# Optimization experiments

Measured on AMD Instinct MI355X. Metric: run time of the kernel, lower is better.

The kernel has to match this reference:

```python
import jax, jax.numpy as jnp
import numpy as np

N = 20000
E = 320000
F_IN = 50
HID = 64          # hidden_channels
HEADS = 8
WIDTH = HID * HEADS  # 512
NUM_CLASSES = 121


def setup_inputs() -> dict:
    key = jax.random.key(0)
    ks = jax.random.split(key, 16)
    def p(k, shape, fan_in):
        return (jax.random.normal(k, shape, dtype=jnp.float32) / np.sqrt(fan_in)).astype(jnp.float32)
    x = jax.random.normal(ks[0], (N, F_IN), dtype=jnp.float32)
    edge_index = jax.random.randint(ks[1], (2, E), 0, N, dtype=jnp.int64)
    return {
        "x": x,
        "edge_index": edge_index,
        # layer 1: 50 -> 64, heads=8, concat
        "W1": p(ks[2], (F_IN, HEADS * HID), F_IN),
        "a1_src": p(ks[3], (HEADS, HID), HID),
        "a1_dst": p(ks[4], (HEADS, HID), HID),
        "b1": jnp.zeros((HEADS * HID,), jnp.float32),
        # layer 2: 512 -> 512, heads=1, concat
        "W2": p(ks[5], (WIDTH, WIDTH), WIDTH),
        "a2_src": p(ks[6], (1, WIDTH), WIDTH),
        "a2_dst": p(ks[7], (1, WIDTH), WIDTH),
        "b2": jnp.zeros((WIDTH,), jnp.float32),
        # layer 3: 512 -> 121, heads=1, concat=False (mean)
        "W3": p(ks[8], (WIDTH, NUM_CLASSES), WIDTH),
        "a3_src": p(ks[9], (1, NUM_CLASSES), NUM_CLASSES),
        "a3_dst": p(ks[10], (1, NUM_CLASSES), NUM_CLASSES),
        "b3": jnp.zeros((NUM_CLASSES,), jnp.float32),
    }


def gat_conv(x, src, dst, W, a_src, a_dst, b, heads, out_ch, concat):
    n = x.shape[0]
    h = (x @ W).reshape(n, heads, out_ch)                 # [N, H, C]
    al_s = jnp.sum(h * a_src, axis=-1)                     # [N, H]
    al_d = jnp.sum(h * a_dst, axis=-1)                     # [N, H]
    e = jax.nn.leaky_relu(al_s[src] + al_d[dst], 0.2)      # [E, H]
    # edge softmax per destination node (stable)
    m = jax.ops.segment_max(e, dst, num_segments=n)        # [N, H]
    m = jnp.where(jnp.isfinite(m), m, 0.0)
    ex = jnp.exp(e - m[dst])
    z = jax.ops.segment_sum(ex, dst, num_segments=n)       # [N, H]
    alpha = ex / (z[dst] + 1e-16)                          # [E, H]
    msg = h[src] * alpha[..., None]                        # [E, H, C]
    out = jax.ops.segment_sum(msg, dst, num_segments=n)    # [N, H, C]
    out = out.reshape(n, heads * out_ch) if concat else out.mean(axis=1)
    return out + b


def reference(x, edge_index, W1, a1_src, a1_dst, b1, W2, a2_src, a2_dst, b2, W3, a3_src, a3_dst, b3):
    n = x.shape[0]
    # PyG GATConv adds self loops by default
    loops = jnp.arange(n, dtype=edge_index.dtype)
    src = jnp.concatenate([edge_index[0], loops])
    dst = jnp.concatenate([edge_index[1], loops])
    # eval mode: dropout is identity
    x1 = gat_conv(x, src, dst, W1, a1_src, a1_dst, b1, HEADS, HID, True)
    h = jax.nn.elu(x1)
    x1 = gat_conv(h, src, dst, W2, a2_src, a2_dst, b2, 1, WIDTH, True)
    h = jax.nn.elu(x1)
    x1 = gat_conv(h, src, dst, W3, a3_src, a3_dst, b3, 1, NUM_CLASSES, False)
    return x1
```

## Files before the change

kernel.cpp:

```cpp
#include <hip/hip_runtime.h>
#include <hip/hip_bf16.h>
#include <hip/hip_fp16.h>

#define NN     20000
#define ERAW   320000
#define ETOT   (ERAW + NN)
#define F_IN   50
#define HID    64
#define HEADS  8
#define WIDTH  512
#define NCLS   121
#define NCLS_P 128

typedef __attribute__((ext_vector_type(8))) __bf16 bf16x8;
typedef __attribute__((ext_vector_type(4))) float floatx4;

__device__ __forceinline__ unsigned short f32_to_bf16_rn(float f) {
  unsigned u = __float_as_uint(f);
  unsigned r = u + 0x7fffu + ((u >> 16) & 1u);
  return (unsigned short)(r >> 16);
}
__device__ __forceinline__ void split_one(float f, unsigned short& h,
                                          unsigned short& l) {
  h = f32_to_bf16_rn(f);
  float fh = __uint_as_float(((unsigned)h) << 16);
  l = f32_to_bf16_rn(f - fh);
}

__device__ __forceinline__ float2 u2f2(unsigned u) {
  __half2 hv = *reinterpret_cast<__half2*>(&u);
  return __half22float2(hv);
}

__device__ __forceinline__ void gll16(const unsigned short* g,
                                      const unsigned short* l) {
  __builtin_amdgcn_global_load_lds(
      (const __attribute__((address_space(1))) unsigned int*)(const void*)g,
      (__attribute__((address_space(3))) unsigned int*)(void*)l, 16, 0, 0);
}

#define PW_BLOCKS 449
__global__ __launch_bounds__(256) void prep_weights(
    const float* __restrict__ W1, const float* __restrict__ W2,
    const float* __restrict__ W3, const float* __restrict__ a1s,
    const float* __restrict__ a1d, unsigned short* __restrict__ w1hHi,
    unsigned short* __restrict__ w1hLo, unsigned short* __restrict__ w2tHi,
    unsigned short* __restrict__ w2tLo, unsigned short* __restrict__ w3tHi,
    unsigned short* __restrict__ w3tLo, float* __restrict__ w1as,
    float* __restrict__ w1ad) {
  __shared__ float t[32][33];
  const int b = blockIdx.x;
  if (b < 320) {
    const float* W;
    unsigned short *thi, *tlo;
    int M, Mp, bx, by;
    const int K = WIDTH;
    if (b < 256) {
      W = W2; thi = w2tHi; tlo = w2tLo; M = WIDTH; Mp = WIDTH;
      bx = b & 15; by = b >> 4;
    } else {
      int bb = b - 256;
      W = W3; thi = w3tHi; tlo = w3tLo; M = NCLS; Mp = NCLS_P;
      bx = bb & 15; by = bb >> 4;
    }
    int k0 = bx * 32, m0 = by * 32;
    int tx = threadIdx.x & 31, ty = threadIdx.x >> 5;
    #pragma unroll
    for (int r = 0; r < 4; ++r) {
      int k = k0 + ty + r * 8, m = m0 + tx;
      float v = 0.f;
      if (k < K && m < M) v = W[(size_t)k * M + m];
      t[ty + r * 8][tx] = v;
    }
    __syncthreads();
    #pragma unroll
    for (int r = 0; r < 4; ++r) {
      int m = m0 + ty + r * 8, k = k0 + tx;
      if (m < Mp && k < K) {
        unsigned short h, l;
        split_one(t[tx][ty + r * 8], h, l);
        thi[(size_t)m * K + k] = h;
        tlo[(size_t)m * K + k] = l;
      }
    }
  } else if (b < 448) {
    int idx = (b - 320) * 256 + threadIdx.x;
    if (idx < HEADS * HID * HID) {
      int hd = idx >> 12, rem = idx & 4095;
      int col = rem >> 6, k = rem & 63;
      float v = (k < F_IN) ? W1[(size_t)k * WIDTH + hd * HID + col] : 0.f;
      unsigned short h, l;
      split_one(v, h, l);
      w1hHi[idx] = h;
      w1hLo[idx] = l;
    }
  } else {
    for (int idx = threadIdx.x; idx < 2 * F_IN * HEADS; idx += 256) {
      int which = idx >= F_IN * HEADS;
      int r = which ? idx - F_IN * HEADS : idx;
      int k = r >> 3, h = r & 7;
      const float* a = which ? a1d : a1s;
      float s = 0.f;
      for (int c = 0; c < HID; ++c)
        s += W1[(size_t)k * WIDTH + h * HID + c] * a[h * HID + c];
      (which ? w1ad : w1as)[r] = s;
    }
  }
}

template <int MI>
__global__ __launch_bounds__(512) void gemm_split_db(
    const unsigned short* __restrict__ Ahi, const unsigned short* __restrict__ Alo,
    const unsigned short* __restrict__ Bthi, const unsigned short* __restrict__ Btlo,
    __half* __restrict__ C16, int N, int K, int M, int Mp, int RB, int CB) {
  constexpr int ABUF = MI * 2048;
  constexpr int BHALF = MI * 4096;
  constexpr int BUF = MI * 4096 + 16384;
  constexpr int NGW = (MI * 8 + 32) / 8;
  __shared__ unsigned short lds[2 * BUF];

  const int f = blockIdx.x;
  const int xcd = f & 7;
  const int g = f >> 3;
  const int cb = g % CB;
  const int rb = (g / CB) * 8 + xcd;
  if (rb >= RB) return;
  const int r0 = rb * (MI * 32), c0 = cb * 128;

  const int tid = threadIdx.x;
  const int wave = tid >> 6, lane = tid & 63;
  const int wr = wave >> 2, wc = wave & 3;
  const int lkg = lane >> 4, lmn = lane & 15;

  const int row8 = lane >> 3, cslot = lane & 7;
  const unsigned short* gsrc[NGW];
  int ldsoff[NGW];
  #pragma unroll
  for (int i = 0; i < NGW; ++i) {
    int q = wave * NGW + i;
    int a, rg;
    if (q < MI * 4)      { a = 0; rg = q; }
    else if (q < MI * 8) { a = 1; rg = q - MI * 4; }
    else { int qb = q - MI * 8; a = 2 + (qb >> 4); rg = qb & 15; }
    int r = rg * 8 + row8;
    int c = cslot ^ (r & 7);
    const unsigned short* base =
        (a == 0) ? Ahi : (a == 1) ? Alo : (a == 2) ? Bthi : Btlo;
    size_t grow;
    if (a < 2) {
      int ra = r0 + r;
      if (ra > N - 1) ra = N - 1;
      grow = (size_t)ra;
    } else {
      grow = (size_t)(c0 + r);
    }
    gsrc[i] = base + grow * K + c * 8;
    int aoff = (a == 0) ? 0 : (a == 1) ? ABUF : (a == 2) ? BHALF
                                              : (BHALF + 8192);
    ldsoff[i] = aoff + rg * 512;
  }

  int rowA[MI], m7A[MI], rowB[2], m7B[2];
  #pragma unroll
  for (int mi = 0; mi < MI; ++mi) {
    int m = wr * (MI * 16) + mi * 16 + lmn;
    rowA[mi] = m * 64;  m7A[mi] = m & 7;
  }
  #pragma unroll
  for (int ni = 0; ni < 2; ++ni) {
    int n = wc * 32 + ni * 16 + lmn;
    rowB[ni] = BHALF + n * 64;  m7B[ni] = n & 7;
  }

  floatx4 acc[MI][2] = {};

  #pragma unroll
  for (int i = 0; i < NGW; ++i) gll16(gsrc[i], lds + ldsoff[i]);

  const int nk = K >> 6;
  for (int t = 0; t < nk; ++t) {
    if (t + 1 < nk) {
      const unsigned short* dst = lds + ((t + 1) & 1) * BUF;
      #pragma unroll
      for (int i = 0; i < NGW; ++i)
        gll16(gsrc[i] + (t + 1) * 64, dst + ldsoff[i]);
      if constexpr (MI == 4) {
        asm volatile("s_waitcnt vmcnt(8)" ::: "memory");
      } else {
        asm volatile("s_waitcnt vmcnt(6)" ::: "memory");
      }
    } else {
      asm volatile("s_waitcnt vmcnt(0)" ::: "memory");
    }
    __builtin_amdgcn_sched_barrier(0);
    __builtin_amdgcn_s_barrier();
    __builtin_amdgcn_sched_barrier(0);

    const unsigned short* Lb = lds + (t & 1) * BUF;
    #pragma unroll
    for (int ksub = 0; ksub < 2; ++ksub) {
      bf16x8 fAhi[MI], fAlo[MI], fBhi[2], fBlo[2];
      #pragma unroll
      for (int mi = 0; mi < MI; ++mi) {
        int s = rowA[mi] + (((ksub << 2) | lkg) ^ m7A[mi]) * 8;
        fAhi[mi] = *(const bf16x8*)(Lb + s);
        fAlo[mi] = *(const bf16x8*)(Lb + s + ABUF);
      }
      #pragma unroll
      for (int ni = 0; ni < 2; ++ni) {
        int s = rowB[ni] + (((ksub << 2) | lkg) ^ m7B[ni]) * 8;
        fBhi[ni] = *(const bf16x8*)(Lb + s);
        fBlo[ni] = *(const bf16x8*)(Lb + s + 8192);
      }
      #pragma unroll
      for (int mi = 0; mi < MI; ++mi)
        #pragma unroll
        for (int ni = 0; ni < 2; ++ni) {
          acc[mi][ni] = __builtin_amdgcn_mfma_f32_16x16x32_bf16(
              fAhi[mi], fBhi[ni], acc[mi][ni], 0, 0, 0);
          acc[mi][ni] = __builtin_amdgcn_mfma_f32_16x16x32_bf16(
              fAhi[mi], fBlo[ni], acc[mi][ni], 0, 0, 0);
          acc[mi][ni] = __builtin_amdgcn_mfma_f32_16x16x32_bf16(
              fAlo[mi], fBhi[ni], acc[mi][ni], 0, 0, 0);
        }
    }

    __builtin_amdgcn_sched_barrier(0);
    asm volatile("s_waitcnt lgkmcnt(0)" ::: "memory");
    __builtin_amdgcn_s_barrier();
    __builtin_amdgcn_sched_barrier(0);
  }

  #pragma unroll
  for (int mi = 0; mi < MI; ++mi) {
    #pragma unroll
    for (int r = 0; r < 4; ++r) {
      int grow = r0 + wr * (MI * 16) + mi * 16 + lkg * 4 + r;
      if (grow >= N) continue;
      #pragma unroll
      for (int ni = 0; ni < 2; ++ni) {
        int gcol = c0 + wc * 32 + ni * 16 + lmn;
        float v = (gcol < M) ? acc[mi][ni][r] : 0.f;
        C16[(size_t)grow * Mp + gcol] = __float2half(v);
      }
    }
  }
}

__global__ __launch_bounds__(256) void gemm_l1_heads(
    const unsigned short* __restrict__ Ahi, const unsigned short* __restrict__ Alo,
    const unsigned short* __restrict__ Bthi, const unsigned short* __restrict__ Btlo,
    unsigned short* __restrict__ outHi, unsigned short* __restrict__ outLo,
    const float* __restrict__ bias) {
  __shared__ unsigned short sAhi[8192], sAlo[8192], sBhi[4096], sBlo[4096];
  const int tid = threadIdx.x;
  const int wave = tid >> 6, lane = tid & 63;
  const int r0 = blockIdx.x * 128;
  const int hd = blockIdx.y;
  const int lkg = lane >> 4, lmn = lane & 15;

  #pragma unroll
  for (int t = 0; t < 4; ++t) {
    int cid = tid + t * 256;
    int row = cid >> 3, c = cid & 7;
    int gr = r0 + row; if (gr > NN - 1) gr = NN - 1;
    const size_t goff = (size_t)gr * WIDTH + hd * HID + c * 8;
    int loff = (((c >> 2) * 4 + (c & 3)) * 128 + row) * 8;
    *(uint4*)(sAhi + loff) = *(const uint4*)(Ahi + goff);
    *(uint4*)(sAlo + loff) = *(const uint4*)(Alo + goff);
  }
  #pragma unroll
  for (int t = 0; t < 2; ++t) {
    int cid = tid + t * 256;
    int col = cid >> 3, c = cid & 7;
    const size_t goff = (size_t)(hd * HID + col) * HID + c * 8;
    int loff = (((c >> 2) * 4 + (c & 3)) * 64 + col) * 8;
    *(uint4*)(sBhi + loff) = *(const uint4*)(Bthi + goff);
    *(uint4*)(sBlo + loff) = *(const uint4*)(Btlo + goff);
  }
  __syncthreads();

  floatx4 acc[2][4] = {};
  #pragma unroll
  for (int ks = 0; ks < 2; ++ks) {
    bf16x8 fAhi[2], fAlo[2], fBhi[4], fBlo[4];
    #pragma unroll
    for (int mi = 0; mi < 2; ++mi) {
      int m = wave * 32 + mi * 16 + lmn;
      int off = ((ks * 4 + lkg) * 128 + m) * 8;
      fAhi[mi] = *(const bf16x8*)(sAhi + off);
      fAlo[mi] = *(const bf16x8*)(sAlo + off);
    }
    #pragma unroll
    for (int ni = 0; ni < 4; ++ni) {
      int n = ni * 16 + lmn;
      int off = ((ks * 4 + lkg) * 64 + n) * 8;
      fBhi[ni] = *(const bf16x8*)(sBhi + off);
      fBlo[ni] = *(const bf16x8*)(sBlo + off);
    }
    #pragma unroll
    for (int mi = 0; mi < 2; ++mi)
      #pragma unroll
      for (int ni = 0; ni < 4; ++ni) {
        acc[mi][ni] = __builtin_amdgcn_mfma_f32_16x16x32_bf16(
            fAhi[mi], fBhi[ni], acc[mi][ni], 0, 0, 0);
        acc[mi][ni] = __builtin_amdgcn_mfma_f32_16x16x32_bf16(
            fAhi[mi], fBlo[ni], acc[mi][ni], 0, 0, 0);
        acc[mi][ni] = __builtin_amdgcn_mfma_f32_16x16x32_bf16(
            fAlo[mi], fBhi[ni], acc[mi][ni], 0, 0, 0);
      }
  }

  #pragma unroll
  for (int mi = 0; mi < 2; ++mi) {
    #pragma unroll
    for (int r = 0; r < 4; ++r) {
      int grow = r0 + wave * 32 + mi * 16 + (lane >> 4) * 4 + r;
      if (grow >= NN) continue;
      #pragma unroll
      for (int ni = 0; ni < 4; ++ni) {
        int gcol = hd * HID + ni * 16 + lmn;
        float v = acc[mi][ni][r] + bias[gcol];
        v = (v > 0.f) ? v : (__expf(v) - 1.0f);
        unsigned short hh, ll;
        split_one(v, hh, ll);
        outHi[(size_t)grow * WIDTH + gcol] = hh;
        outLo[(size_t)grow * WIDTH + gcol] = ll;
      }
    }
  }
}

__global__ __launch_bounds__(256) void al1_kernel(
    const float* __restrict__ x, const float* __restrict__ w1as,
    const float* __restrict__ w1ad, float* __restrict__ al_s,
    float* __restrict__ al_d) {
  int n = (blockIdx.x * blockDim.x + threadIdx.x) >> 6;
  int lane = threadIdx.x & 63;
  if (n >= NN) return;
  float xv = (lane < F_IN) ? x[(size_t)n * F_IN + lane] : 0.f;
  float ws[HEADS], wd[HEADS];
  #pragma unroll
  for (int h = 0; h < HEADS; ++h) {
    ws[h] = (lane < F_IN) ? w1as[lane * HEADS + h] : 0.f;
    wd[h] = (lane < F_IN) ? w1ad[lane * HEADS + h] : 0.f;
  }
  #pragma unroll
  for (int h = 0; h < HEADS; ++h) {
    float ss = xv * ws[h], sd = xv * wd[h];
    #pragma unroll
    for (int o = 32; o; o >>= 1) {
      ss += __shfl_xor(ss, o);
      sd += __shfl_xor(sd, o);
    }
    if (lane == 0) {
      al_s[n * HEADS + h] = ss;
      al_d[n * HEADS + h] = sd;
    }
  }
}

template <int C, int CS>
__global__ __launch_bounds__(256) void compute_al16(
    const __half* __restrict__ h16, const float* __restrict__ a_src,
    const float* __restrict__ a_dst, float* __restrict__ al_s,
    float* __restrict__ al_d) {
  int n = (blockIdx.x * blockDim.x + threadIdx.x) >> 6;
  int lane = threadIdx.x & 63;
  if (n >= NN) return;
  const __half* hr = h16 + (size_t)n * CS;
  float ss = 0.f, sd = 0.f;
  if (C % 512 == 0) {
    uint4 raw = *(const uint4*)(hr + lane * 8);
    float f[8];
    float2 t;
    t = u2f2(raw.x); f[0] = t.x; f[1] = t.y;
    t = u2f2(raw.y); f[2] = t.x; f[3] = t.y;
    t = u2f2(raw.z); f[4] = t.x; f[5] = t.y;
    t = u2f2(raw.w); f[6] = t.x; f[7] = t.y;
    #pragma unroll
    for (int j = 0; j < 8; ++j) {
      int c = lane * 8 + j;
      ss += f[j] * a_src[c];
      sd += f[j] * a_dst[c];
    }
  } else {
    for (int c = lane; c < C; c += 64) {
      float v = __half2float(hr[c]);
      ss += v * a_src[c];
      sd += v * a_dst[c];
    }
  }
  #pragma unroll
  for (int o = 32; o; o >>= 1) {
    ss += __shfl_xor(ss, o);
    sd += __shfl_xor(sd, o);
  }
  if (lane == 0) {
    al_s[n] = ss;
    al_d[n] = sd;
  }
}

__global__ __launch_bounds__(256) void count_deg(
    const int* __restrict__ edst, int* __restrict__ deg) {
  int e = blockIdx.x * blockDim.x + threadIdx.x;
  if (e >= ETOT) return;
  int d = (e < ERAW) ? edst[e] : (e - ERAW);
  atomicAdd(&deg[d], 1);
}

__global__ __launch_bounds__(1024) void scan_deg(
    const int* __restrict__ deg, int* __restrict__ rowptr) {
  __shared__ int part[1024];
  const int t = threadIdx.x;
  const int CHUNK = (NN + 1023) / 1024;
  int lo = t * CHUNK, hi = min(lo + CHUNK, NN);
  int s = 0;
  for (int i = lo; i < hi; ++i) s += deg[i];
  part[t] = s;
  __syncthreads();
  for (int off = 1; off < 1024; off <<= 1) {
    int v = (t >= off) ? part[t - off] : 0;
    __syncthreads();
    part[t] += v;
    __syncthreads();
  }
  int base = (t == 0) ? 0 : part[t - 1];
  for (int i = lo; i < hi; ++i) {
    rowptr[i] = base;
    base += deg[i];
  }
  if (t == 1023) rowptr[NN] = part[1023];
}

__global__ __launch_bounds__(256) void scatter_csr(
    const int* __restrict__ esrc, const int* __restrict__ edst,
    const int* __restrict__ rowptr, int* __restrict__ cnt,
    int* __restrict__ csrc) {
  int e = blockIdx.x * blockDim.x + threadIdx.x;
  if (e >= ETOT) return;
  int s, d;
  if (e < ERAW) { s = esrc[e]; d = edst[e]; }
  else          { s = e - ERAW; d = e - ERAW; }
  int pos = rowptr[d] + atomicAdd(&cnt[d], 1);
  csrc[pos] = s;
}

__global__ __launch_bounds__(256) void agg_x_sm(
    const int* __restrict__ rowptr, const int* __restrict__ csrc,
    const float* __restrict__ al_s, const float* __restrict__ al_d,
    const float* __restrict__ x, unsigned short* __restrict__ outHi,
    unsigned short* __restrict__ outLo) {
  const int w = threadIdx.x >> 6, lane = threadIdx.x & 63;
  const int d = blockIdx.x * 4 + w;
  if (d >= NN) return;
  const int r0 = rowptr[d], r1 = rowptr[d + 1];
  const int mh = lane & 7;
  const float ald_my = al_d[d * HEADS + mh];
  float m_my = al_s[d * HEADS + mh] + ald_my;
  m_my = (m_my > 0.f) ? m_my : 0.2f * m_my;

  float z_my = 0.f;
  float acc[HEADS];
  #pragma unroll
  for (int hh = 0; hh < HEADS; ++hh) acc[hh] = 0.f;

  int p = r0;
  for (; p + 8 <= r1; p += 8) {
    int s[8];
    #pragma unroll
    for (int j = 0; j < 8; ++j) s[j] = csrc[p + j];
    float xv[8];
    #pragma unroll
    for (int j = 0; j < 8; ++j)
      xv[j] = (lane < F_IN) ? x[(size_t)s[j] * F_IN + lane] : 0.f;
    float av[8];
    #pragma unroll
    for (int j = 0; j < 8; ++j) av[j] = al_s[s[j] * HEADS + mh];
    #pragma unroll
    for (int j = 0; j < 8; ++j) {
      float v = av[j] + ald_my;
      v = (v > 0.f) ? v : 0.2f * v;
      float a = __expf(v - m_my);
      z_my += a;
      #pragma unroll
      for (int hh = 0; hh < HEADS; ++hh) acc[hh] += __shfl(a, hh, 8) * xv[j];
    }
  }
  for (; p < r1; ++p) {
    int s = csrc[p];
    float v = al_s[s * HEADS + mh] + ald_my;
    v = (v > 0.f) ? v : 0.2f * v;
    float a = __expf(v - m_my);
    z_my += a;
    float xv = (lane < F_IN) ? x[(size_t)s * F_IN + lane] : 0.f;
    #pragma unroll
    for (int hh = 0; hh < HEADS; ++hh) acc[hh] += __shfl(a, hh, 8) * xv;
  }

  #pragma unroll
  for (int hh = 0; hh < HEADS; ++hh) {
    float zh = __shfl(z_my, hh, 8);
    float v = (lane < F_IN) ? acc[hh] / (zh + 1e-16f) : 0.f;
    unsigned short h2, l2;
    split_one(v, h2, l2);
    outHi[(size_t)d * WIDTH + hh * HID + lane] = h2;
    outLo[(size_t)d * WIDTH + hh * HID + lane] = l2;
  }
}

template <int M, int MS, bool ELU, bool SPLIT>
__global__ __launch_bounds__(256) void pull_agg_sm(
    const int* __restrict__ rowptr, const int* __restrict__ csrc,
    const float* __restrict__ al_s, const float* __restrict__ al_d,
    const __half* __restrict__ h16, const float* __restrict__ bias,
    float* __restrict__ out, unsigned short* __restrict__ outHi,
    unsigned short* __restrict__ outLo) {
  constexpr int EPL = MS / 64;
  const int w = threadIdx.x >> 6;
  const int lane = threadIdx.x & 63;
  const int d = blockIdx.x * 4 + w;
  if (d >= NN) return;
  const int r0 = rowptr[d], r1 = rowptr[d + 1];
  const float ald = al_d[d];
  float m = al_s[d] + ald;
  m = (m > 0.f) ? m : 0.2f * m;

  const int base = lane * EPL;
  const __half* hb = h16 + base;
  float acc[EPL];
  #pragma unroll
  for (int j = 0; j < EPL; ++j) acc[j] = 0.f;
  float z = 0.f;

  int p = r0;
  for (; p + 8 <= r1; p += 8) {
    int s[8];
    #pragma unroll
    for (int j = 0; j < 8; ++j) s[j] = csrc[p + j];
    uint4 raw8[8];
    unsigned raw2[8];
    #pragma unroll
    for (int j = 0; j < 8; ++j) {
      const __half* hr = hb + (size_t)s[j] * MS;
      if (EPL == 8)      raw8[j] = *(const uint4*)hr;
      else if (EPL == 2) raw2[j] = *(const unsigned*)hr;
    }
    float av[8];
    #pragma unroll
    for (int j = 0; j < 8; ++j) av[j] = al_s[s[j]];
    #pragma unroll
    for (int j = 0; j < 8; ++j) {
      float v = av[j] + ald;
      v = (v > 0.f) ? v : 0.2f * v;
      float a = __expf(v - m);
      z += a;
      if (EPL == 8) {
        float2 f0 = u2f2(raw8[j].x), f1 = u2f2(raw8[j].y);
        float2 f2 = u2f2(raw8[j].z), f3 = u2f2(raw8[j].w);
        acc[0] += f0.x * a; acc[1] += f0.y * a;
        acc[2] += f1.x * a; acc[3] += f1.y * a;
        acc[4] += f2.x * a; acc[5] += f2.y * a;
        acc[6] += f3.x * a; acc[7] += f3.y * a;
      } else if (EPL == 2) {
        float2 f0 = u2f2(raw2[j]);
        acc[0] += f0.x * a;
        acc[1] += f0.y * a;
      }
    }
  }
  for (; p < r1; ++p) {
    int s = csrc[p];
    float v = al_s[s] + ald;
    v = (v > 0.f) ? v : 0.2f * v;
    float a = __expf(v - m);
    z += a;
    const __half* hr = hb + (size_t)s * MS;
    if (EPL == 8) {
      uint4 raw = *(const uint4*)hr;
      float2 f0 = u2f2(raw.x), f1 = u2f2(raw.y);
      float2 f2 = u2f2(raw.z), f3 = u2f2(raw.w);
      acc[0] += f0.x * a; acc[1] += f0.y * a;
      acc[2] += f1.x * a; acc[3] += f1.y * a;
      acc[4] += f2.x * a; acc[5] += f2.y * a;
      acc[6] += f3.x * a; acc[7] += f3.y * a;
    } else if (EPL == 2) {
      unsigned raw = *(const unsigned*)hr;
      float2 f0 = u2f2(raw);
      acc[0] += f0.x * a;
      acc[1] += f0.y * a;
    }
  }
  const float iz = 1.0f / (z + 1e-16f);

  #pragma unroll
  for (int j = 0; j < EPL; ++j) {
    if ((M == MS) || (base + j < M)) {
      float v = acc[j] * iz + bias[base + j];
      if (ELU) v = (v > 0.f) ? v : (__expf(v) - 1.0f);
      if (SPLIT) {
        unsigned short hh, ll;
        split_one(v, hh, ll);
        outHi[(size_t)d * M + base + j] = hh;
        outLo[(size_t)d * M + base + j] = ll;
      } else {
        out[(size_t)d * M + base + j] = v;
      }
    }
  }
}

extern "C" void kernel_launch(void* const* d_in, const int* in_sizes, int n_in,
                              void* d_out, int out_size, void* d_ws,
                              size_t ws_size, hipStream_t stream) {
  const float* x      = (const float*)d_in[0];
  const int*   ei     = (const int*)d_in[1];
  const float* W1     = (const float*)d_in[2];
  const float* a1_src = (const float*)d_in[3];
  const float* a1_dst = (const float*)d_in[4];
  const float* b1     = (const float*)d_in[5];
  const float* W2     = (const float*)d_in[6];
  const float* a2_src = (const float*)d_in[7];
  const float* a2_dst = (const float*)d_in[8];
  const float* b2     = (const float*)d_in[9];
  const float* W3     = (const float*)d_in[10];
  const float* a3_src = (const float*)d_in[11];
  const float* a3_dst = (const float*)d_in[12];
  const float* b3     = (const float*)d_in[13];
  float* out = (float*)d_out;

  const int* esrc = ei;
  const int* edst = ei + ERAW;

  unsigned short* p1Hi  = (unsigned short*)d_ws;
  unsigned short* p1Lo  = p1Hi + (size_t)NN * WIDTH;
  unsigned short* p2Hi  = p1Lo + (size_t)NN * WIDTH;
  unsigned short* p2Lo  = p2Hi + (size_t)NN * WIDTH;
  __half*        h16    = (__half*)(p2Lo + (size_t)NN * WIDTH);
  unsigned short* w1hHi = (unsigned short*)(h16 + (size_t)NN * WIDTH);
  unsigned short* w1hLo = w1hHi + (size_t)HEADS * HID * HID;
  unsigned short* w2tHi = w1hLo + (size_t)HEADS * HID * HID;
  unsigned short* w2tLo = w2tHi + (size_t)WIDTH * WIDTH;
  unsigned short* w3tHi = w2tLo + (size_t)WIDTH * WIDTH;
  unsigned short* w3tLo = w3tHi + (size_t)NCLS_P * WIDTH;
  float* al_s   = (float*)(w3tLo + (size_t)NCLS_P * WIDTH);
  float* al_d   = al_s + (size_t)NN * HEADS;
  float* w1as   = al_d + (size_t)NN * HEADS;
  float* w1ad   = w1as + F_IN * HEADS;
  int* deg      = (int*)(w1ad + F_IN * HEADS);
  int* cnt      = deg + NN;
  int* rowptr   = cnt + NN;
  int* csrc     = rowptr + NN + 4;

  hipMemsetAsync(deg, 0, (size_t)(2 * NN) * sizeof(int), stream);
  const int eblk = (ETOT + 255) / 256;
  count_deg<<<eblk, 256, 0, stream>>>(edst, deg);
  scan_deg<<<1, 1024, 0, stream>>>(deg, rowptr);
  scatter_csr<<<eblk, 256, 0, stream>>>(esrc, edst, rowptr, cnt, csrc);

  prep_weights<<<PW_BLOCKS, 256, 0, stream>>>(
      W1, W2, W3, a1_src, a1_dst, w1hHi, w1hLo, w2tHi, w2tLo, w3tHi, w3tLo,
      w1as, w1ad);

  const int nwblk = (NN + 3) / 4;

  al1_kernel<<<nwblk, 256, 0, stream>>>(x, w1as, w1ad, al_s, al_d);
  agg_x_sm<<<nwblk, 256, 0, stream>>>(rowptr, csrc, al_s, al_d, x, p1Hi,
                                      p1Lo);
  gemm_l1_heads<<<dim3((NN + 127) / 128, HEADS), 256, 0, stream>>>(
      p1Hi, p1Lo, w1hHi, w1hLo, p2Hi, p2Lo, b1);

  const int RB2 = (NN + 127) / 128;
  const int G2 = ((RB2 + 7) / 8) * 8 * (WIDTH / 128);
  gemm_split_db<4><<<G2, 512, 0, stream>>>(
      p2Hi, p2Lo, w2tHi, w2tLo, h16, NN, WIDTH, WIDTH, WIDTH, RB2,
      WIDTH / 128);
  compute_al16<WIDTH, WIDTH><<<nwblk, 256, 0, stream>>>(h16, a2_src, a2_dst,
                                                        al_s, al_d);
  pull_agg_sm<WIDTH, WIDTH, true, true><<<nwblk, 256, 0, stream>>>(
      rowptr, csrc, al_s, al_d, h16, b2, nullptr, p1Hi, p1Lo);

  const int RB3 = (NN + 63) / 64;
  const int G3 = ((RB3 + 7) / 8) * 8 * (NCLS_P / 128);
  gemm_split_db<2><<<G3, 512, 0, stream>>>(
      p1Hi, p1Lo, w3tHi, w3tLo, h16, NN, WIDTH, NCLS, NCLS_P, RB3,
      NCLS_P / 128);
  compute_al16<NCLS, NCLS_P><<<nwblk, 256, 0, stream>>>(h16, a3_src, a3_dst,
                                                        al_s, al_d);
  pull_agg_sm<NCLS, NCLS_P, false, false><<<nwblk, 256, 0, stream>>>(
      rowptr, csrc, al_s, al_d, h16, b3, out, nullptr, nullptr);
}
```

Measured before the change: 390.6 us.

## Pad edge loops to batches of 8 and split final aggregation into half-wave rows

The scalar remainder loops in the three pull-aggregation kernels are replaced by a masked batch of 8, with indices clamped to the last edge and weights zeroed, so every neighbor gather is issued in a batched, unrolled group. The templated aggregation kernel is split into a wide variant for layer 2 and a narrow variant for layer 3. The narrow variant maps two destination nodes per wavefront, 32 lanes each with 4 halves per lane, where the old version used 2 per lane. This doubles the destinations handled per wave and cuts idle lanes for the 128-wide output. Masked tail slots cost redundant loads and exp evaluations.

```diff
diff --git a/kernel.cpp b/kernel.cpp
--- a/kernel.cpp
+++ b/kernel.cpp
@@ -466,11 +466,13 @@
   #pragma unroll
   for (int hh = 0; hh < HEADS; ++hh) acc[hh] = 0.f;
 
-  int p = r0;
-  for (; p + 8 <= r1; p += 8) {
+  for (int p = r0; p < r1; p += 8) {
     int s[8];
     #pragma unroll
-    for (int j = 0; j < 8; ++j) s[j] = csrc[p + j];
+    for (int j = 0; j < 8; ++j) {
+      int pj = p + j; if (pj > r1 - 1) pj = r1 - 1;
+      s[j] = csrc[pj];
+    }
     float xv[8];
     #pragma unroll
     for (int j = 0; j < 8; ++j)
@@ -483,20 +485,11 @@
       float v = av[j] + ald_my;
       v = (v > 0.f) ? v : 0.2f * v;
       float a = __expf(v - m_my);
+      if (p + j >= r1) a = 0.f;
       z_my += a;
       #pragma unroll
       for (int hh = 0; hh < HEADS; ++hh) acc[hh] += __shfl(a, hh, 8) * xv[j];
     }
-  }
-  for (; p < r1; ++p) {
-    int s = csrc[p];
-    float v = al_s[s * HEADS + mh] + ald_my;
-    v = (v > 0.f) ? v : 0.2f * v;
-    float a = __expf(v - m_my);
-    z_my += a;
-    float xv = (lane < F_IN) ? x[(size_t)s * F_IN + lane] : 0.f;
-    #pragma unroll
-    for (int hh = 0; hh < HEADS; ++hh) acc[hh] += __shfl(a, hh, 8) * xv;
   }
 
   #pragma unroll
@@ -510,14 +503,11 @@
   }
 }
 
-template <int M, int MS, bool ELU, bool SPLIT>
-__global__ __launch_bounds__(256) void pull_agg_sm(
+__global__ __launch_bounds__(256) void pull_agg_w(
     const int* __restrict__ rowptr, const int* __restrict__ csrc,
     const float* __restrict__ al_s, const float* __restrict__ al_d,
     const __half* __restrict__ h16, const float* __restrict__ bias,
-    float* __restrict__ out, unsigned short* __restrict__ outHi,
-    unsigned short* __restrict__ outLo) {
-  constexpr int EPL = MS / 64;
+    unsigned short* __restrict__ outHi, unsigned short* __restrict__ outLo) {
   const int w = threadIdx.x >> 6;
   const int lane = threadIdx.x & 63;
   const int d = blockIdx.x * 4 + w;
@@ -527,26 +517,24 @@
   float m = al_s[d] + ald;
   m = (m > 0.f) ? m : 0.2f * m;
 
-  const int base = lane * EPL;
+  const int base = lane * 8;
   const __half* hb = h16 + base;
-  float acc[EPL];
-  #pragma unroll
-  for (int j = 0; j < EPL; ++j) acc[j] = 0.f;
+  float acc[8];
+  #pragma unroll
+  for (int j = 0; j < 8; ++j) acc[j] = 0.f;
   float z = 0.f;
 
-  int p = r0;
-  for (; p + 8 <= r1; p += 8) {
+  for (int p = r0; p < r1; p += 8) {
     int s[8];
     #pragma unroll
-    for (int j = 0; j < 8; ++j) s[j] = csrc[p + j];
+    for (int j = 0; j < 8; ++j) {
+      int pj = p + j; if (pj > r1 - 1) pj = r1 - 1;
+      s[j] = csrc[pj];
+    }
     uint4 raw8[8];
-    unsigned raw2[8];
-    #pragma unroll
-    for (int j = 0; j < 8; ++j) {
-      const __half* hr = hb + (size_t)s[j] * MS;
-      if (EPL == 8)      raw8[j] = *(const uint4*)hr;
-      else if (EPL == 2) raw2[j] = *(const unsigned*)hr;
-    }
+    #pragma unroll
+    for (int j = 0; j < 8; ++j)
+      raw8[j] = *(const uint4*)(hb + (size_t)s[j] * WIDTH);
     float av[8];
     #pragma unroll
     for (int j = 0; j < 8; ++j) av[j] = al_s[s[j]];
@@ -555,59 +543,81 @@
       float v = av[j] + ald;
       v = (v > 0.f) ? v : 0.2f * v;
       float a = __expf(v - m);
+      if (p + j >= r1) a = 0.f;
       z += a;
-      if (EPL == 8) {
-        float2 f0 = u2f2(raw8[j].x), f1 = u2f2(raw8[j].y);
-        float2 f2 = u2f2(raw8[j].z), f3 = u2f2(raw8[j].w);
-        acc[0] += f0.x * a; acc[1] += f0.y * a;
-        acc[2] += f1.x * a; acc[3] += f1.y * a;
-        acc[4] += f2.x * a; acc[5] += f2.y * a;
-        acc[6] += f3.x * a; acc[7] += f3.y * a;
-      } else if (EPL == 2) {
-        float2 f0 = u2f2(raw2[j]);
-        acc[0] += f0.x * a;
-        acc[1] += f0.y * a;
-      }
-    }
-  }
-  for (; p < r1; ++p) {
-    int s = csrc[p];
-    float v = al_s[s] + ald;
-    v = (v > 0.f) ? v : 0.2f * v;
-    float a = __expf(v - m);
-    z += a;
-    const __half* hr = hb + (size_t)s * MS;
-    if (EPL == 8) {
-      uint4 raw = *(const uint4*)hr;
-      float2 f0 = u2f2(raw.x), f1 = u2f2(raw.y);
-      float2 f2 = u2f2(raw.z), f3 = u2f2(raw.w);
+      float2 f0 = u2f2(raw8[j].x), f1 = u2f2(raw8[j].y);
+      float2 f2 = u2f2(raw8[j].z), f3 = u2f2(raw8[j].w);
       acc[0] += f0.x * a; acc[1] += f0.y * a;
       acc[2] += f1.x * a; acc[3] += f1.y * a;
       acc[4] += f2.x * a; acc[5] += f2.y * a;
       acc[6] += f3.x * a; acc[7] += f3.y * a;
-    } else if (EPL == 2) {
-      unsigned raw = *(const unsigned*)hr;
-      float2 f0 = u2f2(raw);
-      acc[0] += f0.x * a;
-      acc[1] += f0.y * a;
     }
   }
   const float iz = 1.0f / (z + 1e-16f);
 
   #pragma unroll
-  for (int j = 0; j < EPL; ++j) {
-    if ((M == MS) || (base + j < M)) {
-      float v = acc[j] * iz + bias[base + j];
-      if (ELU) v = (v > 0.f) ? v : (__expf(v) - 1.0f);
-      if (SPLIT) {
-        unsigned short hh, ll;
-        split_one(v, hh, ll);
-        outHi[(size_t)d * M + base + j] = hh;
-        outLo[(size_t)d * M + base + j] = ll;
-      } else {
-        out[(size_t)d * M + base + j] = v;
-      }
-    }
+  for (int j = 0; j < 8; ++j) {
+    float v = acc[j] * iz + bias[base + j];
+    v = (v > 0.f) ? v : (__expf(v) - 1.0f);
+    unsigned short hh, ll;
+    split_one(v, hh, ll);
+    outHi[(size_t)d * WIDTH + base + j] = hh;
+    outLo[(size_t)d * WIDTH + base + j] = ll;
+  }
+}
+
+__global__ __launch_bounds__(256) void pull_agg_n(
+    const int* __restrict__ rowptr, const int* __restrict__ csrc,
+    const float* __restrict__ al_s, const float* __restrict__ al_d,
+    const __half* __restrict__ h16, const float* __restrict__ bias,
+    float* __restrict__ out) {
+  const int w = threadIdx.x >> 6, lane = threadIdx.x & 63;
+  const int half = lane >> 5, li = lane & 31;
+  const int d = blockIdx.x * 8 + w * 2 + half;
+  if (d >= NN) return;
+  const int r0 = rowptr[d], r1 = rowptr[d + 1];
+  const float ald = al_d[d];
+  float m = al_s[d] + ald;
+  m = (m > 0.f) ? m : 0.2f * m;
+
+  const int base = li * 4;
+  const __half* hb = h16 + base;
+  float acc[4] = {0.f, 0.f, 0.f, 0.f};
+  float z = 0.f;
+
+  for (int p = r0; p < r1; p += 8) {
+    int s[8];
+    #pragma unroll
+    for (int j = 0; j < 8; ++j) {
+      int pj = p + j; if (pj > r1 - 1) pj = r1 - 1;
+      s[j] = csrc[pj];
+    }
+    uint2 raw[8];
+    #pragma unroll
+    for (int j = 0; j < 8; ++j)
+      raw[j] = *(const uint2*)(hb + (size_t)s[j] * NCLS_P);
+    float av[8];
+    #pragma unroll
+    for (int j = 0; j < 8; ++j) av[j] = al_s[s[j]];
+    #pragma unroll
+    for (int j = 0; j < 8; ++j) {
+      float v = av[j] + ald;
+      v = (v > 0.f) ? v : 0.2f * v;
+      float a = __expf(v - m);
+      if (p + j >= r1) a = 0.f;
+      z += a;
+      float2 f0 = u2f2(raw[j].x), f1 = u2f2(raw[j].y);
+      acc[0] += f0.x * a; acc[1] += f0.y * a;
+      acc[2] += f1.x * a; acc[3] += f1.y * a;
+    }
+  }
+  const float iz = 1.0f / (z + 1e-16f);
+
+  #pragma unroll
+  for (int j = 0; j < 4; ++j) {
+    int col = base + j;
+    if (col < NCLS)
+      out[(size_t)d * NCLS + col] = acc[j] * iz + bias[col];
   }
 }
 
@@ -678,8 +688,8 @@
       WIDTH / 128);
   compute_al16<WIDTH, WIDTH><<<nwblk, 256, 0, stream>>>(h16, a2_src, a2_dst,
                                                         al_s, al_d);
-  pull_agg_sm<WIDTH, WIDTH, true, true><<<nwblk, 256, 0, stream>>>(
-      rowptr, csrc, al_s, al_d, h16, b2, nullptr, p1Hi, p1Lo);
+  pull_agg_w<<<nwblk, 256, 0, stream>>>(rowptr, csrc, al_s, al_d, h16, b2,
+                                        p1Hi, p1Lo);
 
   const int RB3 = (NN + 63) / 64;
   const int G3 = ((RB3 + 7) / 8) * 8 * (NCLS_P / 128);
@@ -688,6 +698,6 @@
       NCLS_P / 128);
   compute_al16<NCLS, NCLS_P><<<nwblk, 256, 0, stream>>>(h16, a3_src, a3_dst,
                                                         al_s, al_d);
-  pull_agg_sm<NCLS, NCLS_P, false, false><<<nwblk, 256, 0, stream>>>(
-      rowptr, csrc, al_s, al_d, h16, b3, out, nullptr, nullptr);
-}
+  pull_agg_n<<<(NN + 7) / 8, 256, 0, stream>>>(rowptr, csrc, al_s, al_d, h16,
+                                               b3, out);
+}
```

Measured after the change: 394.0 us. Within noise of the previous version (+0.8%).
